# Optimization experiments

Hardware: AMD Instinct MI355X
Metric: run time of the kernel (lower is better)

The kernel has to match this reference:

```python
import jax, jax.numpy as jnp
import numpy as np

N_NODES = 100000
N_EDGES = 1250000
D_IN = 64
D_OUT = 64


def setup_inputs() -> dict:
    key = jax.random.key(0)
    k_h, k_e, k_src, k_dst, k_w, k_b = jax.random.split(key, 6)
    h = jax.random.normal(k_h, (N_NODES, D_IN), dtype=jnp.float32)
    e = jax.random.normal(k_e, (N_EDGES, 1), dtype=jnp.float32)
    src = jax.random.randint(k_src, (N_EDGES,), 0, N_NODES, dtype=jnp.int64)
    dst = jax.random.randint(k_dst, (N_EDGES,), 0, N_NODES, dtype=jnp.int64)
    W = jax.random.normal(k_w, (D_OUT, D_IN), dtype=jnp.float32) / np.sqrt(D_IN)
    b = jax.random.normal(k_b, (D_OUT,), dtype=jnp.float32) * 0.01
    return {"h": h, "e": e, "src": src, "dst": dst, "W": W, "b": b}


def reference(h, e, src, dst, W, b):
    # u_mul_e: gather source node features and multiply by edge features [E,1] -> [E,D]
    m = h[src] * e
    # fn.sum('m','ft'): scatter-add messages into destination nodes -> [N,D]
    ft = jax.ops.segment_sum(m, dst, num_segments=N_NODES)
    # nn.Linear(input_dim, output_dim)
    return ft @ W.T + b
```

## Files before the change

### kernel.cpp

```cpp
#include <hip/hip_runtime.h>

#define N_NODES 100000
#define N_EDGES 1250000
#define D 64
#define BUCKET_BITS 6
#define BUCKET_SZ 64
#define NBUCK 1563
#define CAP 1024
#define EPT 16
#define EPB (EPT * 256)
#define BIN_BLOCKS ((N_EDGES + EPB - 1) / EPB)


typedef __attribute__((ext_vector_type(8))) short bf16x8;
typedef __attribute__((ext_vector_type(4))) float f32x4;

__device__ __forceinline__ unsigned bf16_rne(float x) {
    unsigned u = __float_as_uint(x);
    return (u + 0x7FFFu + ((u >> 16) & 1u)) >> 16;
}
__device__ __forceinline__ float bf16_to_f(unsigned short v) {
    return __uint_as_float(((unsigned)v) << 16);
}

__device__ __forceinline__ void bf16_split(float x, short& hi, short& lo) {
    unsigned hb = bf16_rne(x);
    float fh = __uint_as_float(hb << 16);
    hi = (short)hb;
    lo = (short)bf16_rne(x - fh);
}

__global__ __launch_bounds__(256) void transform_kernel(const float* __restrict__ h,
                                                        const float* __restrict__ W,
                                                        unsigned short* __restrict__ g16,
                                                        int* __restrict__ gcursor) {
    __shared__ unsigned short sh[64 * D];

    int t = threadIdx.x;
    if (blockIdx.x < 7) {
        int i = blockIdx.x * 256 + t;
        if (i < NBUCK) gcursor[i] = 0;
    }

    int lane = t & 63;
    int w = t >> 6;
    int li = lane & 15;
    int lg = lane >> 4;
    int nodebase = blockIdx.x * 64 + w * 16;

    bf16x8 bhi[4][2], blo[4][2];
#pragma unroll
    for (int nt = 0; nt < 4; ++nt) {
#pragma unroll
        for (int kk = 0; kk < 2; ++kk) {
            const float* wp = W + (nt * 16 + li) * D + kk * 32 + lg * 8;
            float4 w0 = *(const float4*)wp;
            float4 w1 = *(const float4*)(wp + 4);
            float v[8] = {w0.x, w0.y, w0.z, w0.w, w1.x, w1.y, w1.z, w1.w};
            bf16x8 h8, l8;
#pragma unroll
            for (int e = 0; e < 8; ++e) { short a, b; bf16_split(v[e], a, b); h8[e] = a; l8[e] = b; }
            bhi[nt][kk] = h8;
            blo[nt][kk] = l8;
        }
    }

    int arow = nodebase + li;
    if (arow > N_NODES - 1) arow = N_NODES - 1;
    bf16x8 ahi[2], alo[2];
#pragma unroll
    for (int kk = 0; kk < 2; ++kk) {
        const float* hp = h + (long)arow * D + kk * 32 + lg * 8;
        float4 h0 = *(const float4*)hp;
        float4 h1 = *(const float4*)(hp + 4);
        float v[8] = {h0.x, h0.y, h0.z, h0.w, h1.x, h1.y, h1.z, h1.w};
        bf16x8 h8, l8;
#pragma unroll
        for (int e = 0; e < 8; ++e) { short a, b; bf16_split(v[e], a, b); h8[e] = a; l8[e] = b; }
        ahi[kk] = h8;
        alo[kk] = l8;
    }

    f32x4 acc[4];
#pragma unroll
    for (int nt = 0; nt < 4; ++nt) acc[nt] = (f32x4){0.f, 0.f, 0.f, 0.f};
#pragma unroll
    for (int kk = 0; kk < 2; ++kk) {
#pragma unroll
        for (int nt = 0; nt < 4; ++nt) {
            acc[nt] = __builtin_amdgcn_mfma_f32_16x16x32_bf16(ahi[kk], bhi[nt][kk], acc[nt], 0, 0, 0);
            acc[nt] = __builtin_amdgcn_mfma_f32_16x16x32_bf16(ahi[kk], blo[nt][kk], acc[nt], 0, 0, 0);
            acc[nt] = __builtin_amdgcn_mfma_f32_16x16x32_bf16(alo[kk], bhi[nt][kk], acc[nt], 0, 0, 0);
        }
    }

#pragma unroll
    for (int nt = 0; nt < 4; ++nt) {
#pragma unroll
        for (int r = 0; r < 4; ++r) {
            sh[(w * 16 + lg * 4 + r) * D + nt * 16 + li] = (unsigned short)bf16_rne(acc[nt][r]);
        }
    }
    __syncthreads();

    const uint4* s4 = (const uint4*)sh;
    uint4* g4 = (uint4*)(g16 + (long)blockIdx.x * 64 * D);
#pragma unroll
    for (int i = t; i < 512; i += 256) {
        int n = blockIdx.x * 64 + (i >> 3);
        if (n < N_NODES) g4[i] = s4[i];
    }
}

__global__ __launch_bounds__(256) void bin_edges_kernel(const int* __restrict__ src,
                                                        const int* __restrict__ dst,
                                                        const float* __restrict__ e,
                                                        int* __restrict__ gcursor,
                                                        int2* __restrict__ packed) {
    __shared__ int lhist[NBUCK];
    int t = threadIdx.x;
    for (int j = t; j < NBUCK; j += 256) lhist[j] = 0;
    __syncthreads();

    int b[EPT], r[EPT], sv[EPT];
    float ev[EPT];
    int base = blockIdx.x * EPB;
#pragma unroll
    for (int j = 0; j < EPT; ++j) {
        int i = base + j * 256 + t;
        b[j] = -1;
        if (i < N_EDGES) {
            int d = dst[i];
            b[j] = d >> BUCKET_BITS;
            sv[j] = src[i] | ((d & (BUCKET_SZ - 1)) << 20);
            ev[j] = e[i];
            r[j] = atomicAdd(&lhist[b[j]], 1);
        }
    }
    __syncthreads();

    for (int x = t; x < NBUCK; x += 256) {
        int c = lhist[x];
        lhist[x] = (c > 0) ? atomicAdd(&gcursor[x], c) : 0;
    }
    __syncthreads();

#pragma unroll
    for (int j = 0; j < EPT; ++j) {
        if (b[j] >= 0) {
            int pos = lhist[b[j]] + r[j];
            if (pos < CAP) packed[b[j] * CAP + pos] = make_int2(sv[j], __float_as_int(ev[j]));
        }
    }
}

__global__ __launch_bounds__(256) void gather_bucket_kernel(const unsigned short* __restrict__ g16,
                                                            const int2* __restrict__ packed,
                                                            const int* __restrict__ gcursor,
                                                            const float* __restrict__ bias,
                                                            float* __restrict__ out) {
    __shared__ int2 eds[CAP];
    __shared__ int nhist[BUCKET_SZ];
    __shared__ int nbase[BUCKET_SZ];
    __shared__ int ncur[BUCKET_SZ];

    int t = threadIdx.x;
    int bk = blockIdx.x;
    int start = bk * CAP;
    int cnt = gcursor[bk];
    if (cnt > CAP) cnt = CAP;

    if (t < BUCKET_SZ) nhist[t] = 0;
    __syncthreads();

    int2 pa = make_int2(0, 0), pb = pa, pc = pa, pd = pa;
    bool va = t < cnt, vb = t + 256 < cnt, vc = t + 512 < cnt, vd = t + 768 < cnt;
    if (va) pa = packed[start + t];
    if (vb) pb = packed[start + t + 256];
    if (vc) pc = packed[start + t + 512];
    if (vd) pd = packed[start + t + 768];
    if (va) atomicAdd(&nhist[(pa.x >> 20) & (BUCKET_SZ - 1)], 1);
    if (vb) atomicAdd(&nhist[(pb.x >> 20) & (BUCKET_SZ - 1)], 1);
    if (vc) atomicAdd(&nhist[(pc.x >> 20) & (BUCKET_SZ - 1)], 1);
    if (vd) atomicAdd(&nhist[(pd.x >> 20) & (BUCKET_SZ - 1)], 1);
    __syncthreads();

    if (t < BUCKET_SZ) {
        int c = nhist[t];
        int v = c;
#pragma unroll
        for (int off = 1; off < BUCKET_SZ; off <<= 1) {
            int x = __shfl_up(v, off, 64);
            if (t >= off) v += x;
        }
        nbase[t] = v - c;
        ncur[t] = v - c;
    }
    __syncthreads();

    if (va) { int dl = (pa.x >> 20) & (BUCKET_SZ - 1); eds[atomicAdd(&ncur[dl], 1)] = pa; }
    if (vb) { int dl = (pb.x >> 20) & (BUCKET_SZ - 1); eds[atomicAdd(&ncur[dl], 1)] = pb; }
    if (vc) { int dl = (pc.x >> 20) & (BUCKET_SZ - 1); eds[atomicAdd(&ncur[dl], 1)] = pc; }
    if (vd) { int dl = (pd.x >> 20) & (BUCKET_SZ - 1); eds[atomicAdd(&ncur[dl], 1)] = pd; }
    __syncthreads();

    int w = t >> 6;
    int lane = t & 63;
    float bv = bias[lane];
    for (int jj = 0; jj < 16; ++jj) {
        int n = w * 16 + jj;
        int gn = bk * BUCKET_SZ + n;
        int s = nbase[n];
        int c = nhist[n];
        float acc = bv;
        int k = 0;
        for (; k + 8 <= c; k += 8) {
            int2 q0 = eds[s + k + 0], q1 = eds[s + k + 1];
            int2 q2 = eds[s + k + 2], q3 = eds[s + k + 3];
            int2 q4 = eds[s + k + 4], q5 = eds[s + k + 5];
            int2 q6 = eds[s + k + 6], q7 = eds[s + k + 7];
            float g0 = bf16_to_f(g16[(long)(q0.x & 0xFFFFF) * D + lane]);
            float g1 = bf16_to_f(g16[(long)(q1.x & 0xFFFFF) * D + lane]);
            float g2 = bf16_to_f(g16[(long)(q2.x & 0xFFFFF) * D + lane]);
            float g3 = bf16_to_f(g16[(long)(q3.x & 0xFFFFF) * D + lane]);
            float g4 = bf16_to_f(g16[(long)(q4.x & 0xFFFFF) * D + lane]);
            float g5 = bf16_to_f(g16[(long)(q5.x & 0xFFFFF) * D + lane]);
            float g6 = bf16_to_f(g16[(long)(q6.x & 0xFFFFF) * D + lane]);
            float g7 = bf16_to_f(g16[(long)(q7.x & 0xFFFFF) * D + lane]);
            acc += __int_as_float(q0.y) * g0;
            acc += __int_as_float(q1.y) * g1;
            acc += __int_as_float(q2.y) * g2;
            acc += __int_as_float(q3.y) * g3;
            acc += __int_as_float(q4.y) * g4;
            acc += __int_as_float(q5.y) * g5;
            acc += __int_as_float(q6.y) * g6;
            acc += __int_as_float(q7.y) * g7;
        }
        if (k + 4 <= c) {
            int2 q0 = eds[s + k + 0], q1 = eds[s + k + 1];
            int2 q2 = eds[s + k + 2], q3 = eds[s + k + 3];
            float g0 = bf16_to_f(g16[(long)(q0.x & 0xFFFFF) * D + lane]);
            float g1 = bf16_to_f(g16[(long)(q1.x & 0xFFFFF) * D + lane]);
            float g2 = bf16_to_f(g16[(long)(q2.x & 0xFFFFF) * D + lane]);
            float g3 = bf16_to_f(g16[(long)(q3.x & 0xFFFFF) * D + lane]);
            acc += __int_as_float(q0.y) * g0;
            acc += __int_as_float(q1.y) * g1;
            acc += __int_as_float(q2.y) * g2;
            acc += __int_as_float(q3.y) * g3;
            k += 4;
        }
        for (; k < c; ++k) {
            int2 q = eds[s + k];
            acc += __int_as_float(q.y) * bf16_to_f(g16[(long)(q.x & 0xFFFFF) * D + lane]);
        }
        if (gn < N_NODES) out[(long)gn * D + lane] = acc;
    }
}

extern "C" void kernel_launch(void* const* d_in, const int* in_sizes, int n_in,
                              void* d_out, int out_size, void* d_ws, size_t ws_size,
                              hipStream_t stream) {
    const float* h   = (const float*)d_in[0];
    const float* e   = (const float*)d_in[1];
    const int*   src = (const int*)d_in[2];
    const int*   dst = (const int*)d_in[3];
    const float* W   = (const float*)d_in[4];
    const float* b   = (const float*)d_in[5];
    float* out = (float*)d_out;

    char* ws = (char*)d_ws;
    int2*           packed  = (int2*)          (ws);
    int*            gcursor = (int*)           (ws + 12804096);
    unsigned short* g16     = (unsigned short*)(ws + 12810368);

    transform_kernel<<<(N_NODES + 63) / 64, 256, 0, stream>>>(h, W, g16, gcursor);

    bin_edges_kernel<<<BIN_BLOCKS, 256, 0, stream>>>(src, dst, e, gcursor, packed);

    gather_bucket_kernel<<<NBUCK, 256, 0, stream>>>(g16, packed, gcursor, b, out);
}
```

Before: 161.6 us.

## Fuse transform and edge-binning kernels; widen gather blocks to 512 threads

The node transform and the edge binning become one launch, with blocks split by index, so the two independent stages run concurrently instead of back to back. The cursor reset moves to a hipMemsetAsync that runs before the fused launch. The gather kernel now uses 512 threads per bucket, each wave handling 8 nodes instead of 16, which adds parallelism per bucket. The cost is an extra memset op, and shared memory sized for both stages in every fused block, which can lower occupancy.

```diff
diff --git a/kernel.cpp b/kernel.cpp
--- a/kernel.cpp
+++ b/kernel.cpp
@@ -10,6 +10,8 @@
 #define EPT 16
 #define EPB (EPT * 256)
 #define BIN_BLOCKS ((N_EDGES + EPB - 1) / EPB)
+#define TR_BLOCKS ((N_NODES + 63) / 64)
+#define FUSED_BLOCKS (TR_BLOCKS + BIN_BLOCKS)
 
 
 typedef __attribute__((ext_vector_type(8))) short bf16x8;
@@ -30,131 +32,126 @@
     lo = (short)bf16_rne(x - fh);
 }
 
-__global__ __launch_bounds__(256) void transform_kernel(const float* __restrict__ h,
-                                                        const float* __restrict__ W,
-                                                        unsigned short* __restrict__ g16,
-                                                        int* __restrict__ gcursor) {
+__global__ __launch_bounds__(256) void transform_bin_kernel(const float* __restrict__ h,
+                                                            const float* __restrict__ W,
+                                                            unsigned short* __restrict__ g16,
+                                                            const int* __restrict__ src,
+                                                            const int* __restrict__ dst,
+                                                            const float* __restrict__ e,
+                                                            int* __restrict__ gcursor,
+                                                            int2* __restrict__ packed) {
     __shared__ unsigned short sh[64 * D];
+    __shared__ int lhist[NBUCK];
 
     int t = threadIdx.x;
-    if (blockIdx.x < 7) {
-        int i = blockIdx.x * 256 + t;
-        if (i < NBUCK) gcursor[i] = 0;
+
+    if (blockIdx.x < TR_BLOCKS) {
+        int lane = t & 63;
+        int w = t >> 6;
+        int li = lane & 15;
+        int lg = lane >> 4;
+        int nodebase = blockIdx.x * 64 + w * 16;
+
+        bf16x8 bhi[4][2], blo[4][2];
+#pragma unroll
+        for (int nt = 0; nt < 4; ++nt) {
+#pragma unroll
+            for (int kk = 0; kk < 2; ++kk) {
+                const float* wp = W + (nt * 16 + li) * D + kk * 32 + lg * 8;
+                float4 w0 = *(const float4*)wp;
+                float4 w1 = *(const float4*)(wp + 4);
+                float v[8] = {w0.x, w0.y, w0.z, w0.w, w1.x, w1.y, w1.z, w1.w};
+                bf16x8 h8, l8;
+#pragma unroll
+                for (int q = 0; q < 8; ++q) { short a, b; bf16_split(v[q], a, b); h8[q] = a; l8[q] = b; }
+                bhi[nt][kk] = h8;
+                blo[nt][kk] = l8;
+            }
+        }
+
+        int arow = nodebase + li;
+        if (arow > N_NODES - 1) arow = N_NODES - 1;
+        bf16x8 ahi[2], alo[2];
+#pragma unroll
+        for (int kk = 0; kk < 2; ++kk) {
+            const float* hp = h + (long)arow * D + kk * 32 + lg * 8;
+            float4 h0 = *(const float4*)hp;
+            float4 h1 = *(const float4*)(hp + 4);
+            float v[8] = {h0.x, h0.y, h0.z, h0.w, h1.x, h1.y, h1.z, h1.w};
+            bf16x8 h8, l8;
+#pragma unroll
+            for (int q = 0; q < 8; ++q) { short a, b; bf16_split(v[q], a, b); h8[q] = a; l8[q] = b; }
+            ahi[kk] = h8;
+            alo[kk] = l8;
+        }
+
+        f32x4 acc[4];
+#pragma unroll
+        for (int nt = 0; nt < 4; ++nt) acc[nt] = (f32x4){0.f, 0.f, 0.f, 0.f};
+#pragma unroll
+        for (int kk = 0; kk < 2; ++kk) {
+#pragma unroll
+            for (int nt = 0; nt < 4; ++nt) {
+                acc[nt] = __builtin_amdgcn_mfma_f32_16x16x32_bf16(ahi[kk], bhi[nt][kk], acc[nt], 0, 0, 0);
+                acc[nt] = __builtin_amdgcn_mfma_f32_16x16x32_bf16(ahi[kk], blo[nt][kk], acc[nt], 0, 0, 0);
+                acc[nt] = __builtin_amdgcn_mfma_f32_16x16x32_bf16(alo[kk], bhi[nt][kk], acc[nt], 0, 0, 0);
+            }
+        }
+
+#pragma unroll
+        for (int nt = 0; nt < 4; ++nt) {
+#pragma unroll
+            for (int r = 0; r < 4; ++r) {
+                sh[(w * 16 + lg * 4 + r) * D + nt * 16 + li] = (unsigned short)bf16_rne(acc[nt][r]);
+            }
+        }
+        __syncthreads();
+
+        const uint4* s4 = (const uint4*)sh;
+        uint4* g4 = (uint4*)(g16 + (long)blockIdx.x * 64 * D);
+#pragma unroll
+        for (int i = t; i < 512; i += 256) {
+            int n = blockIdx.x * 64 + (i >> 3);
+            if (n < N_NODES) g4[i] = s4[i];
+        }
+    } else {
+        for (int j = t; j < NBUCK; j += 256) lhist[j] = 0;
+        __syncthreads();
+
+        int b[EPT], r[EPT], sv[EPT];
+        float ev[EPT];
+        int base = (blockIdx.x - TR_BLOCKS) * EPB;
+#pragma unroll
+        for (int j = 0; j < EPT; ++j) {
+            int i = base + j * 256 + t;
+            b[j] = -1;
+            if (i < N_EDGES) {
+                int d = dst[i];
+                b[j] = d >> BUCKET_BITS;
+                sv[j] = src[i] | ((d & (BUCKET_SZ - 1)) << 20);
+                ev[j] = e[i];
+                r[j] = atomicAdd(&lhist[b[j]], 1);
+            }
+        }
+        __syncthreads();
+
+        for (int x = t; x < NBUCK; x += 256) {
+            int c = lhist[x];
+            lhist[x] = (c > 0) ? atomicAdd(&gcursor[x], c) : 0;
+        }
+        __syncthreads();
+
+#pragma unroll
+        for (int j = 0; j < EPT; ++j) {
+            if (b[j] >= 0) {
+                int pos = lhist[b[j]] + r[j];
+                if (pos < CAP) packed[b[j] * CAP + pos] = make_int2(sv[j], __float_as_int(ev[j]));
+            }
+        }
     }
-
-    int lane = t & 63;
-    int w = t >> 6;
-    int li = lane & 15;
-    int lg = lane >> 4;
-    int nodebase = blockIdx.x * 64 + w * 16;
-
-    bf16x8 bhi[4][2], blo[4][2];
-#pragma unroll
-    for (int nt = 0; nt < 4; ++nt) {
-#pragma unroll
-        for (int kk = 0; kk < 2; ++kk) {
-            const float* wp = W + (nt * 16 + li) * D + kk * 32 + lg * 8;
-            float4 w0 = *(const float4*)wp;
-            float4 w1 = *(const float4*)(wp + 4);
-            float v[8] = {w0.x, w0.y, w0.z, w0.w, w1.x, w1.y, w1.z, w1.w};
-            bf16x8 h8, l8;
-#pragma unroll
-            for (int e = 0; e < 8; ++e) { short a, b; bf16_split(v[e], a, b); h8[e] = a; l8[e] = b; }
-            bhi[nt][kk] = h8;
-            blo[nt][kk] = l8;
-        }
-    }
-
-    int arow = nodebase + li;
-    if (arow > N_NODES - 1) arow = N_NODES - 1;
-    bf16x8 ahi[2], alo[2];
-#pragma unroll
-    for (int kk = 0; kk < 2; ++kk) {
-        const float* hp = h + (long)arow * D + kk * 32 + lg * 8;
-        float4 h0 = *(const float4*)hp;
-        float4 h1 = *(const float4*)(hp + 4);
-        float v[8] = {h0.x, h0.y, h0.z, h0.w, h1.x, h1.y, h1.z, h1.w};
-        bf16x8 h8, l8;
-#pragma unroll
-        for (int e = 0; e < 8; ++e) { short a, b; bf16_split(v[e], a, b); h8[e] = a; l8[e] = b; }
-        ahi[kk] = h8;
-        alo[kk] = l8;
-    }
-
-    f32x4 acc[4];
-#pragma unroll
-    for (int nt = 0; nt < 4; ++nt) acc[nt] = (f32x4){0.f, 0.f, 0.f, 0.f};
-#pragma unroll
-    for (int kk = 0; kk < 2; ++kk) {
-#pragma unroll
-        for (int nt = 0; nt < 4; ++nt) {
-            acc[nt] = __builtin_amdgcn_mfma_f32_16x16x32_bf16(ahi[kk], bhi[nt][kk], acc[nt], 0, 0, 0);
-            acc[nt] = __builtin_amdgcn_mfma_f32_16x16x32_bf16(ahi[kk], blo[nt][kk], acc[nt], 0, 0, 0);
-            acc[nt] = __builtin_amdgcn_mfma_f32_16x16x32_bf16(alo[kk], bhi[nt][kk], acc[nt], 0, 0, 0);
-        }
-    }
-
-#pragma unroll
-    for (int nt = 0; nt < 4; ++nt) {
-#pragma unroll
-        for (int r = 0; r < 4; ++r) {
-            sh[(w * 16 + lg * 4 + r) * D + nt * 16 + li] = (unsigned short)bf16_rne(acc[nt][r]);
-        }
-    }
-    __syncthreads();
-
-    const uint4* s4 = (const uint4*)sh;
-    uint4* g4 = (uint4*)(g16 + (long)blockIdx.x * 64 * D);
-#pragma unroll
-    for (int i = t; i < 512; i += 256) {
-        int n = blockIdx.x * 64 + (i >> 3);
-        if (n < N_NODES) g4[i] = s4[i];
-    }
-}
-
-__global__ __launch_bounds__(256) void bin_edges_kernel(const int* __restrict__ src,
-                                                        const int* __restrict__ dst,
-                                                        const float* __restrict__ e,
-                                                        int* __restrict__ gcursor,
-                                                        int2* __restrict__ packed) {
-    __shared__ int lhist[NBUCK];
-    int t = threadIdx.x;
-    for (int j = t; j < NBUCK; j += 256) lhist[j] = 0;
-    __syncthreads();
-
-    int b[EPT], r[EPT], sv[EPT];
-    float ev[EPT];
-    int base = blockIdx.x * EPB;
-#pragma unroll
-    for (int j = 0; j < EPT; ++j) {
-        int i = base + j * 256 + t;
-        b[j] = -1;
-        if (i < N_EDGES) {
-            int d = dst[i];
-            b[j] = d >> BUCKET_BITS;
-            sv[j] = src[i] | ((d & (BUCKET_SZ - 1)) << 20);
-            ev[j] = e[i];
-            r[j] = atomicAdd(&lhist[b[j]], 1);
-        }
-    }
-    __syncthreads();
-
-    for (int x = t; x < NBUCK; x += 256) {
-        int c = lhist[x];
-        lhist[x] = (c > 0) ? atomicAdd(&gcursor[x], c) : 0;
-    }
-    __syncthreads();
-
-#pragma unroll
-    for (int j = 0; j < EPT; ++j) {
-        if (b[j] >= 0) {
-            int pos = lhist[b[j]] + r[j];
-            if (pos < CAP) packed[b[j] * CAP + pos] = make_int2(sv[j], __float_as_int(ev[j]));
-        }
-    }
-}
-
-__global__ __launch_bounds__(256) void gather_bucket_kernel(const unsigned short* __restrict__ g16,
+}
+
+__global__ __launch_bounds__(512) void gather_bucket_kernel(const unsigned short* __restrict__ g16,
                                                             const int2* __restrict__ packed,
                                                             const int* __restrict__ gcursor,
                                                             const float* __restrict__ bias,
@@ -173,16 +170,12 @@
     if (t < BUCKET_SZ) nhist[t] = 0;
     __syncthreads();
 
-    int2 pa = make_int2(0, 0), pb = pa, pc = pa, pd = pa;
-    bool va = t < cnt, vb = t + 256 < cnt, vc = t + 512 < cnt, vd = t + 768 < cnt;
+    int2 pa = make_int2(0, 0), pb = pa;
+    bool va = t < cnt, vb = t + 512 < cnt;
     if (va) pa = packed[start + t];
-    if (vb) pb = packed[start + t + 256];
-    if (vc) pc = packed[start + t + 512];
-    if (vd) pd = packed[start + t + 768];
+    if (vb) pb = packed[start + t + 512];
     if (va) atomicAdd(&nhist[(pa.x >> 20) & (BUCKET_SZ - 1)], 1);
     if (vb) atomicAdd(&nhist[(pb.x >> 20) & (BUCKET_SZ - 1)], 1);
-    if (vc) atomicAdd(&nhist[(pc.x >> 20) & (BUCKET_SZ - 1)], 1);
-    if (vd) atomicAdd(&nhist[(pd.x >> 20) & (BUCKET_SZ - 1)], 1);
     __syncthreads();
 
     if (t < BUCKET_SZ) {
@@ -200,15 +193,13 @@
 
     if (va) { int dl = (pa.x >> 20) & (BUCKET_SZ - 1); eds[atomicAdd(&ncur[dl], 1)] = pa; }
     if (vb) { int dl = (pb.x >> 20) & (BUCKET_SZ - 1); eds[atomicAdd(&ncur[dl], 1)] = pb; }
-    if (vc) { int dl = (pc.x >> 20) & (BUCKET_SZ - 1); eds[atomicAdd(&ncur[dl], 1)] = pc; }
-    if (vd) { int dl = (pd.x >> 20) & (BUCKET_SZ - 1); eds[atomicAdd(&ncur[dl], 1)] = pd; }
     __syncthreads();
 
     int w = t >> 6;
     int lane = t & 63;
     float bv = bias[lane];
-    for (int jj = 0; jj < 16; ++jj) {
-        int n = w * 16 + jj;
+    for (int jj = 0; jj < 8; ++jj) {
+        int n = w * 8 + jj;
         int gn = bk * BUCKET_SZ + n;
         int s = nbase[n];
         int c = nhist[n];
@@ -273,9 +264,9 @@
     int*            gcursor = (int*)           (ws + 12804096);
     unsigned short* g16     = (unsigned short*)(ws + 12810368);
 
-    transform_kernel<<<(N_NODES + 63) / 64, 256, 0, stream>>>(h, W, g16, gcursor);
-
-    bin_edges_kernel<<<BIN_BLOCKS, 256, 0, stream>>>(src, dst, e, gcursor, packed);
-
-    gather_bucket_kernel<<<NBUCK, 256, 0, stream>>>(g16, packed, gcursor, b, out);
-}
+    hipMemsetAsync(gcursor, 0, NBUCK * sizeof(int), stream);
+
+    transform_bin_kernel<<<FUSED_BLOCKS, 256, 0, stream>>>(h, W, g16, src, dst, e, gcursor, packed);
+
+    gather_bucket_kernel<<<NBUCK, 512, 0, stream>>>(g16, packed, gcursor, b, out);
+}
```

Measured after the change: 157.9 us. -2.3%, faster.
